# Kernel optimization log

Hardware: AMD Instinct MI355X
Metric: run time of the kernel (lower is better)

The kernel has to match this reference:

```python
import jax, jax.numpy as jnp
import numpy as np

L, H, D, DH, F = 2, 12, 768, 64, 3072
B, T = 2, 2048
LN_EPS = 1e-5


def setup_inputs() -> dict:
    key = jax.random.key(0)
    ks = jax.random.split(key, 16)
    s = 0.02
    inp = {
        "x": jax.random.normal(ks[0], (B, T, D), dtype=jnp.float32),
        "attn_mask": jnp.ones((1, T, T), dtype=jnp.int32),
        # per-layer, per-head QKV projections
        "Wq": jax.random.normal(ks[1], (L, H, D, DH), jnp.float32) * s,
        "bq": jnp.zeros((L, H, DH), jnp.float32),
        "Wk": jax.random.normal(ks[2], (L, H, D, DH), jnp.float32) * s,
        "bk": jnp.zeros((L, H, DH), jnp.float32),
        "Wv": jax.random.normal(ks[3], (L, H, D, DH), jnp.float32) * s,
        "bv": jnp.zeros((L, H, DH), jnp.float32),
        # output projection over concatenated heads
        "Wo": jax.random.normal(ks[4], (L, H * DH, D), jnp.float32) * s,
        "bo": jnp.zeros((L, D), jnp.float32),
        # FFN: LayerNorm -> Linear -> GELU -> Linear
        "ln_g": jnp.ones((L, D), jnp.float32),
        "ln_b": jnp.zeros((L, D), jnp.float32),
        "W1": jax.random.normal(ks[5], (L, D, F), jnp.float32) * s,
        "b1": jnp.zeros((L, F), jnp.float32),
        "W2": jax.random.normal(ks[6], (L, F, D), jnp.float32) * s,
        "b2": jnp.zeros((L, D), jnp.float32),
    }
    return inp


def _layer(x, mask, Wq, bq, Wk, bk, Wv, bv, Wo, bo, ln_g, ln_b, W1, b1, W2, b2):
    # batched multi-head attention (equivalent to per-head loop in source)
    q = jnp.einsum("btd,hde->bhte", x, Wq) + bq[None, :, None, :]
    k = jnp.einsum("btd,hde->bhte", x, Wk) + bk[None, :, None, :]
    v = jnp.einsum("btd,hde->bhte", x, Wv) + bv[None, :, None, :]
    scores = jnp.einsum("bhte,bhse->bhts", q, k) / np.sqrt(DH).astype(np.float32)
    scores = jnp.where(mask[:, None, :, :] == 0, -jnp.inf, scores)
    alpha = jax.nn.softmax(scores, axis=-1)
    attn = jnp.einsum("bhts,bhse->bhte", alpha, v)  # [B,H,T,DH]
    concat = attn.transpose(0, 2, 1, 3).reshape(x.shape[0], x.shape[1], H * DH)
    x = concat @ Wo + bo + x  # attention residual
    # FFN with pre-LayerNorm inside the block, residual around it
    mu = jnp.mean(x, axis=-1, keepdims=True)
    var = jnp.mean(jnp.square(x - mu), axis=-1, keepdims=True)
    h = (x - mu) * jax.lax.rsqrt(var + LN_EPS) * ln_g + ln_b
    h = jax.nn.gelu(h @ W1 + b1, approximate=False) @ W2 + b2
    return h + x


def reference(x, attn_mask, Wq, bq, Wk, bk, Wv, bv, Wo, bo, ln_g, ln_b, W1, b1, W2, b2):
    for l in range(L):
        x = _layer(x, attn_mask,
                   Wq[l], bq[l], Wk[l], bk[l], Wv[l], bv[l],
                   Wo[l], bo[l], ln_g[l], ln_b[l],
                   W1[l], b1[l], W2[l], b2[l])
    return x
```

## Files before the change

### kernel.cpp

```cpp
#include <hip/hip_runtime.h>
#include <math.h>

#define CL 2
#define CH 12
#define CD 768
#define CDH 64
#define CF 3072
#define CB 2
#define CT 2048
#define CBH (CB * CH)
#define CBTCD ((size_t)CB * CT * CD)

typedef __bf16 bf16x8 __attribute__((ext_vector_type(8)));
typedef float f32x4 __attribute__((ext_vector_type(4)));
typedef short s16x4 __attribute__((ext_vector_type(4)));
typedef ushort u16x4 __attribute__((ext_vector_type(4)));

#define QSCALE 0.18033688011112042f

__device__ __forceinline__ ushort f2bf(float f) {
  return __builtin_bit_cast(ushort, (__bf16)f);
}

__device__ __forceinline__ float fexp2(float x) {
  float r;
  asm volatile("v_exp_f32 %0, %1" : "=v"(r) : "v"(x));
  return r;
}

__device__ __forceinline__ float wred_sum(float v) {
#pragma unroll
  for (int o = 32; o > 0; o >>= 1) v += __shfl_xor(v, o);
  return v;
}

__device__ __forceinline__ void gload16(const ushort* g, ushort* l) {
  __builtin_amdgcn_global_load_lds(
      (const __attribute__((address_space(1))) unsigned int*)g,
      (__attribute__((address_space(3))) unsigned int*)l, 16, 0, 0);
}

enum { EPI_BF16 = 1, EPI_BIAS_BF16 = 2, EPI_BIAS_GELU_BF16 = 3, EPI_BIAS_RES_F32 = 4, EPI_BIAS_RES_F32_BF16 = 5, EPI_PART_F32 = 6 };

template <int EPI>
__global__ __launch_bounds__(256) void gemm_k(
    const ushort* __restrict__ A, int lda,
    const ushort* __restrict__ B, int ldb,
    void* __restrict__ Cv, int ldc,
    int K,
    const float* __restrict__ bias,
    const float* __restrict__ res,
    ushort* __restrict__ C2) {
  __shared__ ushort As[2][128 * 32];
  __shared__ ushort Bs[2][128 * 32];
  const int tid = threadIdx.x;
  const int lane = tid & 63;
  const int wave = tid >> 6;
  const int wm = (wave >> 1) * 64;
  const int wn = (wave & 1) * 64;

  const int gx = gridDim.x;
  const int nwg = gx * gridDim.y;
  int wgid = blockIdx.y * gx + blockIdx.x;
  const int cpx = nwg >> 3;
  wgid = (wgid & 7) * cpx + (wgid >> 3);
  const int m0 = (wgid / gx) * 128;
  const int n0 = (wgid % gx) * 128;

  const int lr = lane & 15;
  const int lg = lane >> 4;
  f32x4 acc[4][4] = {};

  const int kz = blockIdx.z * K;
  const ushort* pa = A + (size_t)(m0 + (tid >> 2)) * lda + (tid & 3) * 8 + kz;
  const ushort* pb = B + (size_t)(n0 + (tid >> 2)) * ldb + (tid & 3) * 8 + kz;

  auto stage = [&](int buf, int k0) {
#pragma unroll
    for (int p = 0; p < 2; ++p) {
      gload16(pa + (size_t)p * 64 * lda + k0, &As[buf][wave * 512 + p * 2048]);
      gload16(pb + (size_t)p * 64 * ldb + k0, &Bs[buf][wave * 512 + p * 2048]);
    }
  };

  const int nt = K >> 5;
  stage(0, 0);
  for (int kt = 0; kt < nt; ++kt) {
    const int cur = kt & 1;
    if (kt + 1 < nt) {
      stage(cur ^ 1, (kt + 1) << 5);
      asm volatile("s_waitcnt vmcnt(4)" ::: "memory");
    } else {
      asm volatile("s_waitcnt vmcnt(0)" ::: "memory");
    }
    __builtin_amdgcn_s_barrier();
    __builtin_amdgcn_sched_barrier(0);

    bf16x8 af[4], bfr[4];
#pragma unroll
    for (int f = 0; f < 4; ++f) af[f] = *(const bf16x8*)(&As[cur][(wm + f * 16 + lr) * 32 + lg * 8]);
#pragma unroll
    for (int f = 0; f < 4; ++f) bfr[f] = *(const bf16x8*)(&Bs[cur][(wn + f * 16 + lr) * 32 + lg * 8]);
#pragma unroll
    for (int i = 0; i < 4; ++i)
#pragma unroll
      for (int j = 0; j < 4; ++j)
        acc[i][j] = __builtin_amdgcn_mfma_f32_16x16x32_bf16(af[i], bfr[j], acc[i][j], 0, 0, 0);

    __builtin_amdgcn_sched_barrier(0);
    __builtin_amdgcn_s_barrier();
  }

  const int cr0 = lg * 4;
#pragma unroll
  for (int i = 0; i < 4; ++i) {
#pragma unroll
    for (int j = 0; j < 4; ++j) {
      int col = n0 + wn + j * 16 + lr;
#pragma unroll
      for (int r = 0; r < 4; ++r) {
        int row = m0 + wm + i * 16 + cr0 + r;
        float val = acc[i][j][r];
        size_t offc = (size_t)row * ldc + col;
        if constexpr (EPI == EPI_BF16) {
          ((ushort*)Cv)[offc] = f2bf(val);
        } else if constexpr (EPI == EPI_BIAS_BF16) {
          ((ushort*)Cv)[offc] = f2bf(val + bias[col]);
        } else if constexpr (EPI == EPI_BIAS_GELU_BF16) {
          float x = val + bias[col];
          float gel = 0.5f * x * (1.0f + erff(x * 0.70710678118654752f));
          ((ushort*)Cv)[offc] = f2bf(gel);
        } else if constexpr (EPI == EPI_BIAS_RES_F32) {
          ((float*)Cv)[offc] = val + bias[col] + res[offc];
        } else if constexpr (EPI == EPI_PART_F32) {
          ((float*)Cv)[blockIdx.z * CBTCD + offc] = val;
        } else {
          float o = val + bias[col] + res[offc];
          ((float*)Cv)[offc] = o;
          C2[offc] = f2bf(o);
        }
      }
    }
  }
}

template <bool DUAL>
__global__ __launch_bounds__(256) void reduce2_k(const float* __restrict__ part,
                                                 const float* __restrict__ bias,
                                                 const float* __restrict__ res,
                                                 float* __restrict__ outf,
                                                 ushort* __restrict__ outb) {
  int i = blockIdx.x * 256 + threadIdx.x;
  float4 p0 = ((const float4*)part)[i];
  float4 p1 = ((const float4*)(part + CBTCD))[i];
  float4 rr = ((const float4*)res)[i];
  int col = (i * 4) % CD;
  float4 bb = *(const float4*)(bias + col);
  float4 o;
  o.x = p0.x + p1.x + rr.x + bb.x;
  o.y = p0.y + p1.y + rr.y + bb.y;
  o.z = p0.z + p1.z + rr.z + bb.z;
  o.w = p0.w + p1.w + rr.w + bb.w;
  ((float4*)outf)[i] = o;
  if constexpr (DUAL) {
    ushort4 u;
    u.x = f2bf(o.x); u.y = f2bf(o.y); u.z = f2bf(o.z); u.w = f2bf(o.w);
    ((ushort4*)outb)[i] = u;
  }
}

__global__ __launch_bounds__(256) void flash_k(const ushort* __restrict__ qkv,
                                               const ushort* __restrict__ vt,
                                               const unsigned* __restrict__ mbits,
                                               float* __restrict__ Opart,
                                               float2* __restrict__ ml) {
  const int q0 = blockIdx.x * 64;
  const int bh = blockIdx.y;
  const int z = blockIdx.z;
  const int b = bh / CH, h = bh % CH;
  const int tid = threadIdx.x;
  const int lane = tid & 63;
  const int wave = tid >> 6;
  const int lr = lane & 15;
  const int lg = lane >> 4;
  const int KVH = CT / 2;

  __shared__ ushort Ks[64][72];
  __shared__ ushort Vt[64][72];

  const int qg = q0 + wave * 16 + lr;
  const ushort* qrow = qkv + ((size_t)(b * CT) + qg) * 2304 + h * CDH;
  bf16x8 aq0 = *(const bf16x8*)(qrow + lg * 8);
  bf16x8 aq1 = *(const bf16x8*)(qrow + 32 + lg * 8);

  f32x4 acc[4] = {};
  float m_run = -1e30f, l_run = 0.f;

  const ushort* kbase = qkv + ((size_t)(b * CT) + (size_t)z * KVH) * 2304 + CD + h * CDH;
  const ushort* vbase = vt + (size_t)bh * 64 * CT + (size_t)z * KVH;

  const int r0 = tid >> 3, r1 = 32 + (tid >> 3), cc = (tid & 7) * 8;

  auto ld = [&](int kv0, bf16x8& k0, bf16x8& k1, bf16x8& v0, bf16x8& v1) {
    k0 = *(const bf16x8*)(kbase + (size_t)(kv0 + r0) * 2304 + cc);
    k1 = *(const bf16x8*)(kbase + (size_t)(kv0 + r1) * 2304 + cc);
    v0 = *(const bf16x8*)(vbase + (size_t)r0 * CT + kv0 + cc);
    v1 = *(const bf16x8*)(vbase + (size_t)r1 * CT + kv0 + cc);
  };
  auto st = [&](bf16x8 k0, bf16x8 k1, bf16x8 v0, bf16x8 v1) {
    *(bf16x8*)(&Ks[r0][cc]) = k0;
    *(bf16x8*)(&Ks[r1][cc]) = k1;
    *(bf16x8*)(&Vt[r0][cc]) = v0;
    *(bf16x8*)(&Vt[r1][cc]) = v1;
  };

  auto compute = [&](int kv0) {
    f32x4 stt[4];
    __builtin_amdgcn_s_setprio(1);
#pragma unroll
    for (int j = 0; j < 4; ++j) {
      bf16x8 kf0 = *(const bf16x8*)(&Ks[j * 16 + lr][lg * 8]);
      bf16x8 kf1 = *(const bf16x8*)(&Ks[j * 16 + lr][32 + lg * 8]);
      f32x4 t = {};
      t = __builtin_amdgcn_mfma_f32_16x16x32_bf16(kf0, aq0, t, 0, 0, 0);
      t = __builtin_amdgcn_mfma_f32_16x16x32_bf16(kf1, aq1, t, 0, 0, 0);
      stt[j] = t;
    }
    __builtin_amdgcn_s_setprio(0);

    const int kglob = z * KVH + kv0;
    unsigned w0 = mbits[(size_t)qg * 64 + (kglob >> 5)];
    unsigned w1 = mbits[(size_t)qg * 64 + (kglob >> 5) + 1];
    float tmax = -INFINITY;
    if ((w0 & w1) == 0xFFFFFFFFu) {
#pragma unroll
      for (int j = 0; j < 4; ++j)
#pragma unroll
        for (int r = 0; r < 4; ++r) tmax = fmaxf(tmax, stt[j][r]);
    } else {
#pragma unroll
      for (int j = 0; j < 4; ++j) {
        unsigned w = (j < 2) ? w0 : w1;
#pragma unroll
        for (int r = 0; r < 4; ++r) {
          int bit = (j * 16 + lg * 4 + r) & 31;
          if (((w >> bit) & 1u) == 0u) stt[j][r] = -INFINITY;
          tmax = fmaxf(tmax, stt[j][r]);
        }
      }
    }
    tmax = fmaxf(tmax, __shfl_xor(tmax, 16));
    tmax = fmaxf(tmax, __shfl_xor(tmax, 32));

    if (__any(tmax - m_run > 8.0f)) {
      float mnew = fmaxf(m_run, tmax);
      float sc = fexp2(m_run - mnew);
      m_run = mnew;
      l_run *= sc;
#pragma unroll
      for (int jj = 0; jj < 4; ++jj) {
        acc[jj][0] *= sc; acc[jj][1] *= sc; acc[jj][2] *= sc; acc[jj][3] *= sc;
      }
    }

    s16x4 pf[4];
#pragma unroll
    for (int j = 0; j < 4; ++j) {
      s16x4 pv;
#pragma unroll
      for (int r = 0; r < 4; ++r) {
        float p = fexp2(stt[j][r] - m_run);
        l_run += p;
        pv[r] = (short)f2bf(p);
      }
      pf[j] = pv;
    }

    __builtin_amdgcn_s_setprio(1);
#pragma unroll
    for (int jj = 0; jj < 4; ++jj) {
#pragma unroll
      for (int j = 0; j < 4; ++j) {
        s16x4 vf = *(const s16x4*)(&Vt[jj * 16 + lr][j * 16 + lg * 4]);
        acc[jj] = __builtin_amdgcn_mfma_f32_16x16x16bf16_1k(vf, pf[j], acc[jj], 0, 0, 0);
      }
    }
    __builtin_amdgcn_s_setprio(0);
  };

  bf16x8 ka0, ka1, va0, va1, kb0, kb1, vb0, vb1;
  ld(0, ka0, ka1, va0, va1);
  for (int kv0 = 0; kv0 < KVH; kv0 += 128) {
    __syncthreads();
    st(ka0, ka1, va0, va1);
    __syncthreads();
    ld(kv0 + 64, kb0, kb1, vb0, vb1);
    compute(kv0);
    __syncthreads();
    st(kb0, kb1, vb0, vb1);
    __syncthreads();
    if (kv0 + 128 < KVH) ld(kv0 + 128, ka0, ka1, va0, va1);
    compute(kv0 + 64);
  }

  l_run += __shfl_xor(l_run, 16);
  l_run += __shfl_xor(l_run, 32);

  const size_t obase = (((size_t)z * CBH + bh) * CT + qg) * 64;
#pragma unroll
  for (int jj = 0; jj < 4; ++jj)
    *(f32x4*)(Opart + obase + jj * 16 + lg * 4) = acc[jj];
  if (lg == 0) ml[((size_t)z * CBH + bh) * CT + qg] = make_float2(m_run, l_run);
}

__global__ __launch_bounds__(256) void merge_k(const float* __restrict__ Opart,
                                               const float2* __restrict__ ml,
                                               ushort* __restrict__ out) {
  int i = blockIdx.x * 256 + threadIdx.x;
  int e0 = (i & 15) * 4;
  int t = (i >> 4) & (CT - 1);
  int bh = i >> 15;
  int b = bh / CH, h = bh % CH;
  float2 a = ml[(size_t)bh * CT + t];
  float2 c = ml[((size_t)CBH + bh) * CT + t];
  float m = fmaxf(a.x, c.x);
  float w0 = fexp2(a.x - m), w1 = fexp2(c.x - m);
  float inv = 1.0f / (a.y * w0 + c.y * w1);
  float4 o0 = *(const float4*)(Opart + ((size_t)bh * CT + t) * 64 + e0);
  float4 o1 = *(const float4*)(Opart + (((size_t)CBH + bh) * CT + t) * 64 + e0);
  u16x4 o;
  o[0] = f2bf((o0.x * w0 + o1.x * w1) * inv);
  o[1] = f2bf((o0.y * w0 + o1.y * w1) * inv);
  o[2] = f2bf((o0.z * w0 + o1.z * w1) * inv);
  o[3] = f2bf((o0.w * w0 + o1.w * w1) * inv);
  *(u16x4*)(out + ((size_t)b * CT + t) * CD + h * CDH + e0) = o;
}

__global__ __launch_bounds__(256) void vtrans_k(const ushort* __restrict__ qkv,
                                                ushort* __restrict__ vt) {
  const int t0 = blockIdx.x * 64;
  const int bh = blockIdx.y;
  const int b = bh / CH, h = bh % CH;
  const int tid = threadIdx.x;
  __shared__ ushort tile[64][72];
#pragma unroll
  for (int p = 0; p < 2; ++p) {
    int i = p * 2048 + tid * 8;
    int tr = i >> 6, c = i & 63;
    *(bf16x8*)(&tile[tr][c]) =
        *(const bf16x8*)(qkv + (size_t)(b * CT + t0 + tr) * 2304 + 2 * CD + h * CDH + c);
  }
  __syncthreads();
#pragma unroll
  for (int p = 0; p < 2; ++p) {
    int i = p * 2048 + tid * 8;
    int er = i >> 6, tc = i & 63;
    ushort tmp[8];
#pragma unroll
    for (int j = 0; j < 8; ++j) tmp[j] = tile[tc + j][er];
    *(bf16x8*)(vt + (size_t)bh * 64 * CT + (size_t)er * CT + t0 + tc) = *(bf16x8*)tmp;
  }
}

__global__ void maskbits_k(const int* __restrict__ mask, unsigned* __restrict__ mbits) {
  int idx = blockIdx.x * 256 + threadIdx.x;
  if (idx >= CT * 64) return;
  const int* mp = mask + (size_t)(idx >> 6) * CT + (idx & 63) * 32;
  unsigned bits = 0;
#pragma unroll
  for (int j = 0; j < 32; ++j) bits |= (mp[j] != 0 ? 1u : 0u) << j;
  mbits[idx] = bits;
}

__global__ __launch_bounds__(256) void ln_k(const float* __restrict__ X,
                                            ushort* __restrict__ H,
                                            const float* __restrict__ g,
                                            const float* __restrict__ b) {
  const int t = blockIdx.x;
  const int tid = threadIdx.x;
  const float* row = X + (size_t)t * CD;
  float x0 = row[tid], x1 = row[tid + 256], x2 = row[tid + 512];
  float s = wred_sum(x0 + x1 + x2);
  __shared__ float sh[4], sh2[4];
  if ((tid & 63) == 0) sh[tid >> 6] = s;
  __syncthreads();
  float mu = (sh[0] + sh[1] + sh[2] + sh[3]) * (1.0f / 768.0f);
  float d0 = x0 - mu, d1 = x1 - mu, d2 = x2 - mu;
  float vs = wred_sum(d0 * d0 + d1 * d1 + d2 * d2);
  if ((tid & 63) == 0) sh2[tid >> 6] = vs;
  __syncthreads();
  float var = (sh2[0] + sh2[1] + sh2[2] + sh2[3]) * (1.0f / 768.0f);
  float r = 1.0f / sqrtf(var + 1e-5f);
  H[(size_t)t * CD + tid] = f2bf(d0 * r * g[tid] + b[tid]);
  H[(size_t)t * CD + tid + 256] = f2bf(d1 * r * g[tid + 256] + b[tid + 256]);
  H[(size_t)t * CD + tid + 512] = f2bf(d2 * r * g[tid + 512] + b[tid + 512]);
}

__global__ void f32_to_bf16_k(const float* __restrict__ in, ushort* __restrict__ out, int n4) {
  int i = blockIdx.x * 256 + threadIdx.x;
  if (i >= n4) return;
  float4 f = *(const float4*)(in + (size_t)i * 4);
  ushort4 u;
  u.x = f2bf(f.x); u.y = f2bf(f.y); u.z = f2bf(f.z); u.w = f2bf(f.w);
  *(ushort4*)(out + (size_t)i * 4) = u;
}

__global__ __launch_bounds__(256) void tcvt_k(const float* __restrict__ src, size_t sbs,
                                              ushort* __restrict__ dst, size_t dbs,
                                              int R, int C, float scale) {
  __shared__ float t[32][33];
  const float* s = src + blockIdx.z * sbs;
  ushort* d = dst + blockIdx.z * dbs;
  const int tx = threadIdx.x & 31;
  const int ty4 = (threadIdx.x >> 5) * 4;
  const int r0 = blockIdx.y * 32, c0 = blockIdx.x * 32;
#pragma unroll
  for (int i = 0; i < 4; ++i) t[ty4 + i][tx] = s[(size_t)(r0 + ty4 + i) * C + c0 + tx];
  __syncthreads();
#pragma unroll
  for (int i = 0; i < 4; ++i)
    d[(size_t)(c0 + ty4 + i) * R + r0 + tx] = f2bf(t[tx][ty4 + i] * scale);
}

__global__ void repack_bqkv_k(const float* __restrict__ bq, const float* __restrict__ bk,
                              const float* __restrict__ bv, float* __restrict__ dst) {
  int idx = blockIdx.x * 256 + threadIdx.x;
  if (idx >= CL * 2304) return;
  int l = idx / 2304;
  int c = idx % 2304;
  int sec = c / CD;
  int within = c % CD;
  int h = within / CDH;
  int e = within % CDH;
  const float* B = (sec == 0) ? bq : ((sec == 1) ? bk : bv);
  float v = B[((size_t)l * CH + h) * CDH + e];
  if (sec == 0) v *= QSCALE;
  dst[idx] = v;
}

extern "C" void kernel_launch(void* const* d_in, const int* in_sizes, int n_in,
                              void* d_out, int out_size, void* d_ws, size_t ws_size,
                              hipStream_t stream) {
  (void)in_sizes; (void)n_in; (void)out_size; (void)ws_size;
  const float* X = (const float*)d_in[0];
  const int* MSK = (const int*)d_in[1];
  const float* Wq = (const float*)d_in[2];
  const float* bq = (const float*)d_in[3];
  const float* Wk = (const float*)d_in[4];
  const float* bk = (const float*)d_in[5];
  const float* Wv = (const float*)d_in[6];
  const float* bv = (const float*)d_in[7];
  const float* Wo = (const float*)d_in[8];
  const float* bo = (const float*)d_in[9];
  const float* lng = (const float*)d_in[10];
  const float* lnb = (const float*)d_in[11];
  const float* W1 = (const float*)d_in[12];
  const float* b1 = (const float*)d_in[13];
  const float* W2 = (const float*)d_in[14];
  const float* b2 = (const float*)d_in[15];

  char* base = (char*)d_ws;
  size_t off = 0;
  auto alloc = [&](size_t bytes) {
    char* p = base + off;
    off = (off + bytes + 255) & ~(size_t)255;
    return p;
  };
  ushort* wqkv_t = (ushort*)alloc((size_t)CL * 2304 * CD * 2);
  ushort* wo_t = (ushort*)alloc((size_t)CL * CD * CD * 2);
  ushort* w1_t = (ushort*)alloc((size_t)CL * CF * CD * 2);
  ushort* w2_t = (ushort*)alloc((size_t)CL * CD * CF * 2);
  float* bqkv = (float*)alloc((size_t)CL * 2304 * 4);
  ushort* xb = (ushort*)alloc((size_t)CB * CT * CD * 2);
  ushort* qkv = (ushort*)alloc((size_t)CB * CT * 2304 * 2);
  ushort* vt = (ushort*)alloc((size_t)CB * CH * CDH * CT * 2);
  unsigned* mbits = (unsigned*)alloc((size_t)CT * 64 * 4);
  ushort* attno = (ushort*)alloc((size_t)CB * CT * CD * 2);
  float* xattn = (float*)alloc((size_t)CB * CT * CD * 4);
  float* xf = (float*)alloc((size_t)CB * CT * CD * 4);
  ushort* hln = (ushort*)alloc((size_t)CB * CT * CD * 2);
  ushort* gbuf = (ushort*)alloc((size_t)CB * CT * CF * 2);
  float2* ml = (float2*)alloc((size_t)2 * CBH * CT * 8);
  float* part = (float*)qkv;
  float* Opart = (float*)gbuf;

  const int BT_ = CB * CT;

  for (int l = 0; l < CL; ++l) {
    tcvt_k<<<dim3(CDH / 32, CD / 32, CH), 256, 0, stream>>>(
        Wq + (size_t)l * CH * CD * CDH, (size_t)CD * CDH,
        wqkv_t + (size_t)l * 2304 * CD + 0 * CD * CD, (size_t)CDH * CD,
        CD, CDH, QSCALE);
    tcvt_k<<<dim3(CDH / 32, CD / 32, CH), 256, 0, stream>>>(
        Wk + (size_t)l * CH * CD * CDH, (size_t)CD * CDH,
        wqkv_t + (size_t)l * 2304 * CD + 1 * CD * CD, (size_t)CDH * CD,
        CD, CDH, 1.0f);
    tcvt_k<<<dim3(CDH / 32, CD / 32, CH), 256, 0, stream>>>(
        Wv + (size_t)l * CH * CD * CDH, (size_t)CD * CDH,
        wqkv_t + (size_t)l * 2304 * CD + 2 * CD * CD, (size_t)CDH * CD,
        CD, CDH, 1.0f);
  }
  tcvt_k<<<dim3(CD / 32, CD / 32, CL), 256, 0, stream>>>(
      Wo, (size_t)CD * CD, wo_t, (size_t)CD * CD, CD, CD, 1.0f);
  tcvt_k<<<dim3(CF / 32, CD / 32, CL), 256, 0, stream>>>(
      W1, (size_t)CD * CF, w1_t, (size_t)CF * CD, CD, CF, 1.0f);
  tcvt_k<<<dim3(CD / 32, CF / 32, CL), 256, 0, stream>>>(
      W2, (size_t)CF * CD, w2_t, (size_t)CD * CF, CF, CD, 1.0f);
  {
    int n = CL * 2304;
    repack_bqkv_k<<<(n + 255) / 256, 256, 0, stream>>>(bq, bk, bv, bqkv);
  }
  maskbits_k<<<(CT * 64 + 255) / 256, 256, 0, stream>>>(MSK, mbits);

  {
    int n4 = BT_ * CD / 4;
    f32_to_bf16_k<<<(n4 + 255) / 256, 256, 0, stream>>>(X, xb, n4);
  }

  for (int l = 0; l < CL; ++l) {
    const float* xcur = (l == 0) ? X : xf;
    gemm_k<EPI_BIAS_BF16><<<dim3(2304 / 128, BT_ / 128), 256, 0, stream>>>(
        xb, CD, wqkv_t + (size_t)l * 2304 * CD, CD, qkv, 2304, CD,
        bqkv + (size_t)l * 2304, nullptr, nullptr);
    vtrans_k<<<dim3(CT / 64, CBH), 256, 0, stream>>>(qkv, vt);
    flash_k<<<dim3(CT / 64, CBH, 2), 256, 0, stream>>>(qkv, vt, mbits, Opart, ml);
    merge_k<<<CBH * CT * 16 / 256, 256, 0, stream>>>(Opart, ml, attno);
    gemm_k<EPI_BIAS_RES_F32><<<dim3(CD / 128, BT_ / 128), 256, 0, stream>>>(
        attno, CD, wo_t + (size_t)l * CD * CD, CD, xattn, CD, CD,
        bo + (size_t)l * CD, xcur, nullptr);
    ln_k<<<BT_, 256, 0, stream>>>(xattn, hln, lng + (size_t)l * CD, lnb + (size_t)l * CD);
    gemm_k<EPI_BIAS_GELU_BF16><<<dim3(CF / 128, BT_ / 128), 256, 0, stream>>>(
        hln, CD, w1_t + (size_t)l * CF * CD, CD, gbuf, CF, CD,
        b1 + (size_t)l * CF, nullptr, nullptr);
    gemm_k<EPI_PART_F32><<<dim3(CD / 128, BT_ / 128, 2), 256, 0, stream>>>(
        gbuf, CF, w2_t + (size_t)l * CD * CF, CF, part, CD, CF / 2,
        nullptr, nullptr, nullptr);
    const int nred = BT_ * CD / 4 / 256;
    if (l == CL - 1) {
      reduce2_k<false><<<nred, 256, 0, stream>>>(part, b2 + (size_t)l * CD, xattn,
                                                 (float*)d_out, nullptr);
    } else {
      reduce2_k<true><<<nred, 256, 0, stream>>>(part, b2 + (size_t)l * CD, xattn,
                                                xf, xb);
    }
  }
}
```

Before: 453.6 us.

## Double query rows per wave in flash kernel with async swizzled LDS staging

Each wave now handles two 16-row query tiles (128 queries per block), so every K/V tile loaded into shared memory feeds twice the MFMA work. Staging switches from register round-trips to direct global-to-LDS loads (gload16) into an XOR-swizzled, double-buffered layout, with explicit vmcnt waits and raw barriers in place of the previous syncthreads pairs. The swizzle is meant to avoid LDS bank conflicts without padding. In exchange the block count is halved, lowering occupancy and parallelism, and register pressure rises from the second set of accumulators.

```diff
diff --git a/kernel.cpp b/kernel.cpp
--- a/kernel.cpp
+++ b/kernel.cpp
@@ -174,7 +174,7 @@
                                                const unsigned* __restrict__ mbits,
                                                float* __restrict__ Opart,
                                                float2* __restrict__ ml) {
-  const int q0 = blockIdx.x * 64;
+  const int q0 = blockIdx.x * 128;
   const int bh = blockIdx.y;
   const int z = blockIdx.z;
   const int b = bh / CH, h = bh % CH;
@@ -185,58 +185,51 @@
   const int lg = lane >> 4;
   const int KVH = CT / 2;
 
-  __shared__ ushort Ks[64][72];
-  __shared__ ushort Vt[64][72];
-
-  const int qg = q0 + wave * 16 + lr;
-  const ushort* qrow = qkv + ((size_t)(b * CT) + qg) * 2304 + h * CDH;
-  bf16x8 aq0 = *(const bf16x8*)(qrow + lg * 8);
-  bf16x8 aq1 = *(const bf16x8*)(qrow + 32 + lg * 8);
-
-  f32x4 acc[4] = {};
-  float m_run = -1e30f, l_run = 0.f;
+  __shared__ ushort Ks[2][64 * 64];
+  __shared__ ushort Vs[2][64 * 64];
+
+  const int qg0 = q0 + wave * 32 + lr;
+  const int qg1 = qg0 + 16;
+  const ushort* qrow0 = qkv + ((size_t)(b * CT) + qg0) * 2304 + h * CDH;
+  const ushort* qrow1 = qkv + ((size_t)(b * CT) + qg1) * 2304 + h * CDH;
+  bf16x8 aq00 = *(const bf16x8*)(qrow0 + lg * 8);
+  bf16x8 aq01 = *(const bf16x8*)(qrow0 + 32 + lg * 8);
+  bf16x8 aq10 = *(const bf16x8*)(qrow1 + lg * 8);
+  bf16x8 aq11 = *(const bf16x8*)(qrow1 + 32 + lg * 8);
+
+  f32x4 acc0[4] = {}, acc1[4] = {};
+  float m0 = -1e30f, l0 = 0.f, m1 = -1e30f, l1 = 0.f;
 
   const ushort* kbase = qkv + ((size_t)(b * CT) + (size_t)z * KVH) * 2304 + CD + h * CDH;
   const ushort* vbase = vt + (size_t)bh * 64 * CT + (size_t)z * KVH;
 
-  const int r0 = tid >> 3, r1 = 32 + (tid >> 3), cc = (tid & 7) * 8;
-
-  auto ld = [&](int kv0, bf16x8& k0, bf16x8& k1, bf16x8& v0, bf16x8& v1) {
-    k0 = *(const bf16x8*)(kbase + (size_t)(kv0 + r0) * 2304 + cc);
-    k1 = *(const bf16x8*)(kbase + (size_t)(kv0 + r1) * 2304 + cc);
-    v0 = *(const bf16x8*)(vbase + (size_t)r0 * CT + kv0 + cc);
-    v1 = *(const bf16x8*)(vbase + (size_t)r1 * CT + kv0 + cc);
+  const int koff0 = (lg ^ (lr & 7)) * 8;
+  const int koff1 = ((4 + lg) ^ (lr & 7)) * 8;
+  int voff[4];
+#pragma unroll
+  for (int j = 0; j < 4; ++j)
+    voff[j] = (((2 * j + (lg >> 1)) ^ (lr & 7)) * 8) + (lg & 1) * 4;
+
+  const int srow = lane >> 3;
+  const int scol = ((lane & 7) ^ srow) * 8;
+
+  auto stage = [&](int buf, int kv0) {
+#pragma unroll
+    for (int c = 0; c < 2; ++c) {
+      const int rbase = wave * 16 + c * 8;
+      gload16(kbase + (size_t)(kv0 + rbase + srow) * 2304 + scol, &Ks[buf][rbase * 64]);
+      gload16(vbase + (size_t)(rbase + srow) * CT + kv0 + scol, &Vs[buf][rbase * 64]);
+    }
   };
-  auto st = [&](bf16x8 k0, bf16x8 k1, bf16x8 v0, bf16x8 v1) {
-    *(bf16x8*)(&Ks[r0][cc]) = k0;
-    *(bf16x8*)(&Ks[r1][cc]) = k1;
-    *(bf16x8*)(&Vt[r0][cc]) = v0;
-    *(bf16x8*)(&Vt[r1][cc]) = v1;
-  };
-
-  auto compute = [&](int kv0) {
-    f32x4 stt[4];
-    __builtin_amdgcn_s_setprio(1);
-#pragma unroll
-    for (int j = 0; j < 4; ++j) {
-      bf16x8 kf0 = *(const bf16x8*)(&Ks[j * 16 + lr][lg * 8]);
-      bf16x8 kf1 = *(const bf16x8*)(&Ks[j * 16 + lr][32 + lg * 8]);
-      f32x4 t = {};
-      t = __builtin_amdgcn_mfma_f32_16x16x32_bf16(kf0, aq0, t, 0, 0, 0);
-      t = __builtin_amdgcn_mfma_f32_16x16x32_bf16(kf1, aq1, t, 0, 0, 0);
-      stt[j] = t;
-    }
-    __builtin_amdgcn_s_setprio(0);
-
-    const int kglob = z * KVH + kv0;
-    unsigned w0 = mbits[(size_t)qg * 64 + (kglob >> 5)];
-    unsigned w1 = mbits[(size_t)qg * 64 + (kglob >> 5) + 1];
+
+  auto softmax = [&](f32x4 (&st)[4], unsigned w0, unsigned w1, float& m_run,
+                     float& l_run, f32x4 (&acc)[4], s16x4 (&pf)[4]) {
     float tmax = -INFINITY;
     if ((w0 & w1) == 0xFFFFFFFFu) {
 #pragma unroll
       for (int j = 0; j < 4; ++j)
 #pragma unroll
-        for (int r = 0; r < 4; ++r) tmax = fmaxf(tmax, stt[j][r]);
+        for (int r = 0; r < 4; ++r) tmax = fmaxf(tmax, st[j][r]);
     } else {
 #pragma unroll
       for (int j = 0; j < 4; ++j) {
@@ -244,14 +237,13 @@
 #pragma unroll
         for (int r = 0; r < 4; ++r) {
           int bit = (j * 16 + lg * 4 + r) & 31;
-          if (((w >> bit) & 1u) == 0u) stt[j][r] = -INFINITY;
-          tmax = fmaxf(tmax, stt[j][r]);
+          if (((w >> bit) & 1u) == 0u) st[j][r] = -INFINITY;
+          tmax = fmaxf(tmax, st[j][r]);
         }
       }
     }
     tmax = fmaxf(tmax, __shfl_xor(tmax, 16));
     tmax = fmaxf(tmax, __shfl_xor(tmax, 32));
-
     if (__any(tmax - m_run > 8.0f)) {
       float mnew = fmaxf(m_run, tmax);
       float sc = fexp2(m_run - mnew);
@@ -262,55 +254,103 @@
         acc[jj][0] *= sc; acc[jj][1] *= sc; acc[jj][2] *= sc; acc[jj][3] *= sc;
       }
     }
-
-    s16x4 pf[4];
 #pragma unroll
     for (int j = 0; j < 4; ++j) {
       s16x4 pv;
 #pragma unroll
       for (int r = 0; r < 4; ++r) {
-        float p = fexp2(stt[j][r] - m_run);
+        float p = fexp2(st[j][r] - m_run);
         l_run += p;
         pv[r] = (short)f2bf(p);
       }
       pf[j] = pv;
     }
-
+  };
+
+  const int NT = KVH / 64;
+  stage(0, 0);
+  for (int t = 0; t < NT; ++t) {
+    const int cur = t & 1;
+    const int widx = z * 32 + 2 * t;
+    unsigned w00 = mbits[(size_t)qg0 * 64 + widx];
+    unsigned w01 = mbits[(size_t)qg0 * 64 + widx + 1];
+    unsigned w10 = mbits[(size_t)qg1 * 64 + widx];
+    unsigned w11 = mbits[(size_t)qg1 * 64 + widx + 1];
+    if (t + 1 < NT) {
+      stage(cur ^ 1, (t + 1) * 64);
+      asm volatile("s_waitcnt vmcnt(4)" ::: "memory");
+    } else {
+      asm volatile("s_waitcnt vmcnt(0)" ::: "memory");
+    }
+    __builtin_amdgcn_s_barrier();
+    __builtin_amdgcn_sched_barrier(0);
+
+    const ushort* K = &Ks[cur][0];
+    const ushort* V = &Vs[cur][0];
+
+    f32x4 st0[4];
     __builtin_amdgcn_s_setprio(1);
 #pragma unroll
+    for (int j = 0; j < 4; ++j) {
+      bf16x8 kf0 = *(const bf16x8*)(K + (j * 16 + lr) * 64 + koff0);
+      bf16x8 kf1 = *(const bf16x8*)(K + (j * 16 + lr) * 64 + koff1);
+      f32x4 tt = {};
+      tt = __builtin_amdgcn_mfma_f32_16x16x32_bf16(kf0, aq00, tt, 0, 0, 0);
+      tt = __builtin_amdgcn_mfma_f32_16x16x32_bf16(kf1, aq01, tt, 0, 0, 0);
+      st0[j] = tt;
+    }
+    __builtin_amdgcn_s_setprio(0);
+    s16x4 pf0[4];
+    softmax(st0, w00, w01, m0, l0, acc0, pf0);
+
+    f32x4 st1[4];
+    __builtin_amdgcn_s_setprio(1);
+#pragma unroll
+    for (int j = 0; j < 4; ++j) {
+      bf16x8 kf0 = *(const bf16x8*)(K + (j * 16 + lr) * 64 + koff0);
+      bf16x8 kf1 = *(const bf16x8*)(K + (j * 16 + lr) * 64 + koff1);
+      f32x4 tt = {};
+      tt = __builtin_amdgcn_mfma_f32_16x16x32_bf16(kf0, aq10, tt, 0, 0, 0);
+      tt = __builtin_amdgcn_mfma_f32_16x16x32_bf16(kf1, aq11, tt, 0, 0, 0);
+      st1[j] = tt;
+    }
+    __builtin_amdgcn_s_setprio(0);
+    s16x4 pf1[4];
+    softmax(st1, w10, w11, m1, l1, acc1, pf1);
+
+    __builtin_amdgcn_s_setprio(1);
+#pragma unroll
     for (int jj = 0; jj < 4; ++jj) {
+      s16x4 vf[4];
+#pragma unroll
+      for (int j = 0; j < 4; ++j)
+        vf[j] = *(const s16x4*)(V + (jj * 16 + lr) * 64 + voff[j]);
 #pragma unroll
       for (int j = 0; j < 4; ++j) {
-        s16x4 vf = *(const s16x4*)(&Vt[jj * 16 + lr][j * 16 + lg * 4]);
-        acc[jj] = __builtin_amdgcn_mfma_f32_16x16x16bf16_1k(vf, pf[j], acc[jj], 0, 0, 0);
+        acc0[jj] = __builtin_amdgcn_mfma_f32_16x16x16bf16_1k(vf[j], pf0[j], acc0[jj], 0, 0, 0);
+        acc1[jj] = __builtin_amdgcn_mfma_f32_16x16x16bf16_1k(vf[j], pf1[j], acc1[jj], 0, 0, 0);
       }
     }
     __builtin_amdgcn_s_setprio(0);
-  };
-
-  bf16x8 ka0, ka1, va0, va1, kb0, kb1, vb0, vb1;
-  ld(0, ka0, ka1, va0, va1);
-  for (int kv0 = 0; kv0 < KVH; kv0 += 128) {
-    __syncthreads();
-    st(ka0, ka1, va0, va1);
-    __syncthreads();
-    ld(kv0 + 64, kb0, kb1, vb0, vb1);
-    compute(kv0);
-    __syncthreads();
-    st(kb0, kb1, vb0, vb1);
-    __syncthreads();
-    if (kv0 + 128 < KVH) ld(kv0 + 128, ka0, ka1, va0, va1);
-    compute(kv0 + 64);
-  }
-
-  l_run += __shfl_xor(l_run, 16);
-  l_run += __shfl_xor(l_run, 32);
-
-  const size_t obase = (((size_t)z * CBH + bh) * CT + qg) * 64;
-#pragma unroll
-  for (int jj = 0; jj < 4; ++jj)
-    *(f32x4*)(Opart + obase + jj * 16 + lg * 4) = acc[jj];
-  if (lg == 0) ml[((size_t)z * CBH + bh) * CT + qg] = make_float2(m_run, l_run);
+
+    __builtin_amdgcn_sched_barrier(0);
+    __builtin_amdgcn_s_barrier();
+  }
+
+  l0 += __shfl_xor(l0, 16); l0 += __shfl_xor(l0, 32);
+  l1 += __shfl_xor(l1, 16); l1 += __shfl_xor(l1, 32);
+
+  const size_t ob0 = (((size_t)z * CBH + bh) * CT + qg0) * 64;
+  const size_t ob1 = (((size_t)z * CBH + bh) * CT + qg1) * 64;
+#pragma unroll
+  for (int jj = 0; jj < 4; ++jj) {
+    *(f32x4*)(Opart + ob0 + jj * 16 + lg * 4) = acc0[jj];
+    *(f32x4*)(Opart + ob1 + jj * 16 + lg * 4) = acc1[jj];
+  }
+  if (lg == 0) {
+    ml[((size_t)z * CBH + bh) * CT + qg0] = make_float2(m0, l0);
+    ml[((size_t)z * CBH + bh) * CT + qg1] = make_float2(m1, l1);
+  }
 }
 
 __global__ __launch_bounds__(256) void merge_k(const float* __restrict__ Opart,
@@ -523,7 +563,7 @@
         xb, CD, wqkv_t + (size_t)l * 2304 * CD, CD, qkv, 2304, CD,
         bqkv + (size_t)l * 2304, nullptr, nullptr);
     vtrans_k<<<dim3(CT / 64, CBH), 256, 0, stream>>>(qkv, vt);
-    flash_k<<<dim3(CT / 64, CBH, 2), 256, 0, stream>>>(qkv, vt, mbits, Opart, ml);
+    flash_k<<<dim3(CT / 128, CBH, 2), 256, 0, stream>>>(qkv, vt, mbits, Opart, ml);
     merge_k<<<CBH * CT * 16 / 256, 256, 0, stream>>>(Opart, ml, attno);
     gemm_k<EPI_BIAS_RES_F32><<<dim3(CD / 128, BT_ / 128), 256, 0, stream>>>(
         attno, CD, wo_t + (size_t)l * CD * CD, CD, xattn, CD, CD,
```

Result: slower. 475.6 us (+4.8%).
